# Performance work log

Measured on AMD Instinct MI355X. Metric: run time of the kernel, lower is better.

Reference implementation:

```python
import jax, jax.numpy as jnp
import numpy as np

LBDA = 0.5  # soft-min temperature, default in OTAM_cum_dist_v2


def setup_inputs() -> dict:
    key = jax.random.key(0)
    # frame-similarity distances [n_queries, n_support, q_len, s_len];
    # in the repo these are 1 - cos_sim, i.e. small non-negative floats
    dists = jnp.abs(jax.random.normal(key, (256, 64, 48, 48), dtype=jnp.float32))
    return {"dists": dists}


def _otam_cum_dist(dists, lbda=LBDA):
    """Faithful vectorized port of OTAM_cum_dist_v2.

    dists: [nq, ns, L, M] -> returns [nq, ns] = cum_dists[:, :, -1, -1]
    The torch code pads the last dim by (1,1) with zeros, then runs a
    soft-DTW-style DP:
      row 0      : running sum along m
      col 0      : stays 0 (never written for l >= 1)
      m == 1     : softmin(prev[0],   prev[1],   cur[0])
      1 < m < -1 : softmin(prev[m-1], cur[m-1])
      m == -1    : softmin(prev[-2],  prev[-1],  cur[-2])
    with softmin(xs) = -lbda * log(sum(exp(-x/lbda))).
    """
    nq, ns, L, M = dists.shape
    B = nq * ns
    d = dists.reshape(B, L, M)
    d = jnp.pad(d, ((0, 0), (0, 0), (1, 1)))  # [B, L, M2], M2 = M + 2
    M2 = M + 2

    # row 0: cum[0, m] = cum[0, m-1] + d[0, m], cum[0, 0] = 0 (d[...,0] is the pad 0)
    row0 = jnp.cumsum(d[:, 0, :], axis=-1)  # [B, M2]

    m_idx = jnp.arange(1, M2)
    # prev[m] participates in the softmin only at the two edge columns
    incl_prev_m = (m_idx == 1) | (m_idx == M2 - 1)  # [M2-1] bool

    def row_step(prev, d_row):
        # prev, d_row: [B, M2]; sequential recurrence along m (cur[m] needs cur[m-1])
        xs = (d_row[:, 1:].T, prev[:, :-1].T, prev[:, 1:].T, incl_prev_m)

        def cell(c_prev, x):
            d_m, p_m1, p_m, inc = x  # [B] each, inc scalar bool
            p_m_eff = jnp.where(inc, p_m, jnp.inf)  # exp(-inf/lbda) = 0 -> excluded
            cand = jnp.stack([p_m1, c_prev, p_m_eff], axis=0)  # [3, B]
            c = d_m - lbda * jax.nn.logsumexp(-cand / lbda, axis=0)
            return c, c

        c0 = jnp.zeros(prev.shape[0], dtype=prev.dtype)  # cur[l, 0] = 0
        _, cur = jax.lax.scan(cell, c0, xs)  # [M2-1, B]
        cur = jnp.concatenate([c0[None, :], cur], axis=0).T  # [B, M2]
        return cur, None

    d_rows = jnp.swapaxes(d, 0, 1)[1:]  # [L-1, B, M2]
    final, _ = jax.lax.scan(row_step, row0, d_rows)  # [B, M2]
    return final[:, -1].reshape(nq, ns)


def reference(dists):
    return _otam_cum_dist(dists, LBDA)
```

## Files before the change

kernel.cpp:

```cpp
#include <hip/hip_runtime.h>


__global__ __launch_bounds__(64, 1) void otam_kernel(const float* __restrict__ dists,
                                                     float* __restrict__ out) {
    const int b = blockIdx.x * 64 + threadIdx.x;
    const float* __restrict__ dp = dists + (size_t)b * (48 * 48);

    double P[49];

    {
        const float4* __restrict__ r4 = reinterpret_cast<const float4*>(dp);
        double run = 1.0;
#pragma unroll
        for (int v = 0; v < 12; ++v) {
            float4 q = r4[v];
            run *= (double)__expf(-2.0f * q.x); P[4 * v + 0] = run;
            run *= (double)__expf(-2.0f * q.y); P[4 * v + 1] = run;
            run *= (double)__expf(-2.0f * q.z); P[4 * v + 2] = run;
            run *= (double)__expf(-2.0f * q.w); P[4 * v + 3] = run;
        }
        P[48] = run;
    }

    for (int l = 1; l < 48; ++l) {
        const float4* __restrict__ r4 = reinterpret_cast<const float4*>(dp + l * 48);
        float a[48];
#pragma unroll
        for (int v = 0; v < 12; ++v) {
            float4 q = r4[v];
            a[4 * v + 0] = __expf(-2.0f * q.x);
            a[4 * v + 1] = __expf(-2.0f * q.y);
            a[4 * v + 2] = __expf(-2.0f * q.z);
            a[4 * v + 3] = __expf(-2.0f * q.w);
        }

        double c = (double)a[0] * (2.0 + P[0]);

#pragma unroll
        for (int m = 2; m <= 48; ++m) {
            double t = (double)a[m - 1] * (c + P[m - 2]);
            P[m - 2] = c;
            c = t;
        }

        double t = c + P[47] + P[48];
        P[47] = c;
        P[48] = t;
    }

    out[b] = (float)(-0.5 * log(P[48]));
}

extern "C" void kernel_launch(void* const* d_in, const int* in_sizes, int n_in,
                              void* d_out, int out_size, void* d_ws, size_t ws_size,
                              hipStream_t stream) {
    const float* dists = (const float*)d_in[0];
    float* out = (float*)d_out;
    otam_kernel<<<dim3(256), dim3(64), 0, stream>>>(dists, out);
}
```

Baseline: 240.5 us.

## Split each DP row across 8 lanes with a shuffle-based linear-recurrence scan

Instead of one thread walking all 48 columns of a problem, each problem is now handled by 8 lanes that each own 6 columns. The serial row recurrence is written as an affine map and combined with a log-step shuffle scan, and the next row is prefetched into registers. The goal is to raise parallelism from 16384 threads in 256 single-wave blocks to 131072 threads and to shorten the serial dependency chain. The cost is extra double-precision multiplies and shuffles per row, and rescaling no longer happens per element.

```diff
diff --git a/kernel.cpp b/kernel.cpp
--- a/kernel.cpp
+++ b/kernel.cpp
@@ -1,54 +1,91 @@
 #include <hip/hip_runtime.h>
 
 
-__global__ __launch_bounds__(64, 1) void otam_kernel(const float* __restrict__ dists,
-                                                     float* __restrict__ out) {
-    const int b = blockIdx.x * 64 + threadIdx.x;
-    const float* __restrict__ dp = dists + (size_t)b * (48 * 48);
+__global__ __launch_bounds__(256, 2) void otam_kernel(const float* __restrict__ dists,
+                                                      float* __restrict__ out) {
+    const int t = blockIdx.x * 256 + threadIdx.x;
+    const int k = t & 7;
+    const int prob = t >> 3;
+    const int lane = threadIdx.x & 63;
 
-    double P[49];
+    const float* __restrict__ dp = dists + (size_t)prob * (48 * 48) + 6 * k;
 
-    {
-        const float4* __restrict__ r4 = reinterpret_cast<const float4*>(dp);
-        double run = 1.0;
+    double P[6];
+    double F49 = 0.0;
+
+    float2 q0 = *reinterpret_cast<const float2*>(dp + 0);
+    float2 q1 = *reinterpret_cast<const float2*>(dp + 2);
+    float2 q2 = *reinterpret_cast<const float2*>(dp + 4);
+
+    for (int l = 0; l < 48; ++l) {
+        const float d0 = q0.x, d1 = q0.y, d2 = q1.x, d3 = q1.y, d4 = q2.x, d5 = q2.y;
+
+        {
+            const float* np = dp + (l < 47 ? (l + 1) : l) * 48;
+            q0 = *reinterpret_cast<const float2*>(np + 0);
+            q1 = *reinterpret_cast<const float2*>(np + 2);
+            q2 = *reinterpret_cast<const float2*>(np + 4);
+        }
+
+        double al[6], be[6];
+        al[0] = (double)__expf(-2.0f * d0);
+        al[1] = (double)__expf(-2.0f * d1);
+        al[2] = (double)__expf(-2.0f * d2);
+        al[3] = (double)__expf(-2.0f * d3);
+        al[4] = (double)__expf(-2.0f * d4);
+        al[5] = (double)__expf(-2.0f * d5);
+
+        double Pold5 = 0.0;
+        if (l == 0) {
+            be[0] = 0.0; be[1] = 0.0; be[2] = 0.0; be[3] = 0.0; be[4] = 0.0; be[5] = 0.0;
+        } else {
+            double Plast = __shfl(P[5], (lane - 1) & 63);
+            double pfirst = (k == 0) ? (1.0 + P[0]) : Plast;
+            be[0] = al[0] * pfirst;
+            be[1] = al[1] * P[0];
+            be[2] = al[2] * P[1];
+            be[3] = al[3] * P[2];
+            be[4] = al[4] * P[3];
+            be[5] = al[5] * P[4];
+            Pold5 = P[5];
+        }
+
+        double A = al[0], B = be[0];
 #pragma unroll
-        for (int v = 0; v < 12; ++v) {
-            float4 q = r4[v];
-            run *= (double)__expf(-2.0f * q.x); P[4 * v + 0] = run;
-            run *= (double)__expf(-2.0f * q.y); P[4 * v + 1] = run;
-            run *= (double)__expf(-2.0f * q.z); P[4 * v + 2] = run;
-            run *= (double)__expf(-2.0f * q.w); P[4 * v + 3] = run;
+        for (int i = 1; i < 6; ++i) {
+            B = al[i] * B + be[i];
+            A = al[i] * A;
         }
-        P[48] = run;
+
+#pragma unroll
+        for (int s = 1; s <= 4; s <<= 1) {
+            double Ap = __shfl(A, (lane - s) & 63);
+            double Bp = __shfl(B, (lane - s) & 63);
+            Ap = (k >= s) ? Ap : 1.0;
+            Bp = (k >= s) ? Bp : 0.0;
+            B = A * Bp + B;
+            A = A * Ap;
+        }
+
+        double tAB = A + B;
+        double yin = __shfl(tAB, (lane - 1) & 63);
+        yin = (k == 0) ? 1.0 : yin;
+
+        double y = yin;
+#pragma unroll
+        for (int i = 0; i < 6; ++i) {
+            y = al[i] * y + be[i];
+            P[i] = y;
+        }
+
+        if (k == 7) {
+            F49 = (l == 0) ? y : (y + Pold5 + F49);
+        }
     }
 
-    for (int l = 1; l < 48; ++l) {
-        const float4* __restrict__ r4 = reinterpret_cast<const float4*>(dp + l * 48);
-        float a[48];
-#pragma unroll
-        for (int v = 0; v < 12; ++v) {
-            float4 q = r4[v];
-            a[4 * v + 0] = __expf(-2.0f * q.x);
-            a[4 * v + 1] = __expf(-2.0f * q.y);
-            a[4 * v + 2] = __expf(-2.0f * q.z);
-            a[4 * v + 3] = __expf(-2.0f * q.w);
-        }
-
-        double c = (double)a[0] * (2.0 + P[0]);
-
-#pragma unroll
-        for (int m = 2; m <= 48; ++m) {
-            double t = (double)a[m - 1] * (c + P[m - 2]);
-            P[m - 2] = c;
-            c = t;
-        }
-
-        double t = c + P[47] + P[48];
-        P[47] = c;
-        P[48] = t;
+    if (k == 7) {
+        out[prob] = (float)(-0.5 * log(F49));
     }
-
-    out[b] = (float)(-0.5 * log(P[48]));
 }
 
 extern "C" void kernel_launch(void* const* d_in, const int* in_sizes, int n_in,
@@ -56,5 +93,5 @@
                               hipStream_t stream) {
     const float* dists = (const float*)d_in[0];
     float* out = (float*)d_out;
-    otam_kernel<<<dim3(256), dim3(64), 0, stream>>>(dists, out);
+    otam_kernel<<<dim3(512), dim3(256), 0, stream>>>(dists, out);
 }
```

Result: faster. 216.4 us (-10.0%).

## Parallelize each DP row across 16 lanes with shuffle-based linear-recurrence scan

Applied to the files above, without the earlier changes.

Each problem previously ran on a single thread with a serial 48-step double-precision recurrence per row. The new code gives each problem 16 lanes that own 3 columns each. Each row's first-order linear recurrence is solved with a Hillis-Steele scan of (A,B) affine pairs over wavefront shuffles, in float32 with per-row power-of-two rescaling and a tracked exponent offset. It also prefetches the next row's loads and launches 16x more threads. The risks are float32 precision loss, plus the shuffle and rescaling overhead on every row.

```diff
diff --git a/kernel.cpp b/kernel.cpp
--- a/kernel.cpp
+++ b/kernel.cpp
@@ -1,54 +1,105 @@
 #include <hip/hip_runtime.h>
 
 
-__global__ __launch_bounds__(64, 1) void otam_kernel(const float* __restrict__ dists,
-                                                     float* __restrict__ out) {
-    const int b = blockIdx.x * 64 + threadIdx.x;
-    const float* __restrict__ dp = dists + (size_t)b * (48 * 48);
+__global__ __launch_bounds__(256, 4) void otam_kernel(const float* __restrict__ dists,
+                                                      float* __restrict__ out) {
+    const int t = blockIdx.x * 256 + threadIdx.x;
+    const int k = t & 15;
+    const int prob = t >> 4;
+    const int lane = threadIdx.x & 63;
 
-    double P[49];
+    const float* __restrict__ dp = dists + (size_t)prob * (48 * 48) + 3 * k;
+
+    float P0, P1, P2;
+    float F49 = 0.0f;
+    float S = 1.0f;
+    int offE = 0;
+
+    float q0 = dp[0], q1 = dp[1], q2 = dp[2];
 
     {
-        const float4* __restrict__ r4 = reinterpret_cast<const float4*>(dp);
-        double run = 1.0;
+        float a0 = __expf(-2.0f * q0);
+        float a1 = __expf(-2.0f * q1);
+        float a2 = __expf(-2.0f * q2);
+        q0 = dp[48]; q1 = dp[49]; q2 = dp[50];
+
+        float Ap0 = a0, Ap1 = a0 * a1, Ap2 = a0 * a1 * a2;
+        float A = Ap2;
 #pragma unroll
-        for (int v = 0; v < 12; ++v) {
-            float4 q = r4[v];
-            run *= (double)__expf(-2.0f * q.x); P[4 * v + 0] = run;
-            run *= (double)__expf(-2.0f * q.y); P[4 * v + 1] = run;
-            run *= (double)__expf(-2.0f * q.z); P[4 * v + 2] = run;
-            run *= (double)__expf(-2.0f * q.w); P[4 * v + 3] = run;
+        for (int s = 1; s <= 8; s <<= 1) {
+            float Au = __shfl(A, (lane - s) & 63);
+            A *= (k >= s) ? Au : 1.0f;
         }
-        P[48] = run;
+        float yin = __shfl(A, (lane - 1) & 63);
+        yin = (k == 0) ? 1.0f : yin;
+        P0 = Ap0 * yin; P1 = Ap1 * yin; P2 = Ap2 * yin;
+        F49 = P2;
+    }
+
+    {
+        float m = fmaxf(P0, fmaxf(P1, P2));
+#pragma unroll
+        for (int s = 1; s <= 8; s <<= 1) m = fmaxf(m, __shfl_xor(m, s));
+        unsigned e = (__float_as_uint(m) >> 23) & 0xFFu;
+        float sc = __uint_as_float((254u - e) << 23);
+        offE += (int)e - 127;
+        P0 *= sc; P1 *= sc; P2 *= sc; F49 *= sc; S *= sc;
     }
 
     for (int l = 1; l < 48; ++l) {
-        const float4* __restrict__ r4 = reinterpret_cast<const float4*>(dp + l * 48);
-        float a[48];
-#pragma unroll
-        for (int v = 0; v < 12; ++v) {
-            float4 q = r4[v];
-            a[4 * v + 0] = __expf(-2.0f * q.x);
-            a[4 * v + 1] = __expf(-2.0f * q.y);
-            a[4 * v + 2] = __expf(-2.0f * q.z);
-            a[4 * v + 3] = __expf(-2.0f * q.w);
+        float a0 = __expf(-2.0f * q0);
+        float a1 = __expf(-2.0f * q1);
+        float a2 = __expf(-2.0f * q2);
+
+        {
+            const float* np = dp + (l < 47 ? (l + 1) : l) * 48;
+            q0 = np[0]; q1 = np[1]; q2 = np[2];
         }
 
-        double c = (double)a[0] * (2.0 + P[0]);
+        float Plast = __shfl(P2, (lane - 1) & 63);
+        float pfirst = (k == 0) ? (S + P0) : Plast;
+        float be0 = a0 * pfirst;
+        float be1 = a1 * P0;
+        float be2 = a2 * P1;
+        float PoldLast = P2;
 
+        float Ap0 = a0,        Bp0 = be0;
+        float Ap1 = a1 * Ap0,  Bp1 = fmaf(a1, Bp0, be1);
+        float Ap2 = a2 * Ap1,  Bp2 = fmaf(a2, Bp1, be2);
+
+        float A = Ap2, B = Bp2;
 #pragma unroll
-        for (int m = 2; m <= 48; ++m) {
-            double t = (double)a[m - 1] * (c + P[m - 2]);
-            P[m - 2] = c;
-            c = t;
+        for (int s = 1; s <= 8; s <<= 1) {
+            float Au = __shfl(A, (lane - s) & 63);
+            float Bu = __shfl(B, (lane - s) & 63);
+            Au = (k >= s) ? Au : 1.0f;
+            Bu = (k >= s) ? Bu : 0.0f;
+            B = fmaf(A, Bu, B);
+            A *= Au;
         }
 
-        double t = c + P[47] + P[48];
-        P[47] = c;
-        P[48] = t;
+        float incl = fmaf(A, S, B);
+        float yin = __shfl(incl, (lane - 1) & 63);
+        yin = (k == 0) ? S : yin;
+
+        P0 = fmaf(Ap0, yin, Bp0);
+        P1 = fmaf(Ap1, yin, Bp1);
+        P2 = fmaf(Ap2, yin, Bp2);
+
+        if (k == 15) F49 = P2 + PoldLast + F49;
+
+        float m = fmaxf(P0, fmaxf(P1, P2));
+#pragma unroll
+        for (int s = 1; s <= 8; s <<= 1) m = fmaxf(m, __shfl_xor(m, s));
+        unsigned e = (__float_as_uint(m) >> 23) & 0xFFu;
+        float sc = __uint_as_float((254u - e) << 23);
+        offE += (int)e - 127;
+        P0 *= sc; P1 *= sc; P2 *= sc; F49 *= sc; S *= sc;
     }
 
-    out[b] = (float)(-0.5 * log(P[48]));
+    if (k == 15) {
+        out[prob] = -0.5f * (logf(F49) + (float)offE * 0.6931471805599453f);
+    }
 }
 
 extern "C" void kernel_launch(void* const* d_in, const int* in_sizes, int n_in,
@@ -56,5 +107,5 @@
                               hipStream_t stream) {
     const float* dists = (const float*)d_in[0];
     float* out = (float*)d_out;
-    otam_kernel<<<dim3(256), dim3(64), 0, stream>>>(dists, out);
+    otam_kernel<<<dim3(1024), dim3(256), 0, stream>>>(dists, out);
 }
```

Measured after the change: 211.7 us. -11.9%, faster.

## Parallelize DP rows across 16 lanes with DPP affine scan and float renormalization

Applied to the files above, without the earlier changes.

Replaces the one-thread-per-problem double-precision recurrence with 16 lanes per problem. Each lane owns 4 columns, and each row's linear recurrence is solved as an affine prefix scan using DPP row shifts. Precision drops from double to float, with periodic power-of-two renormalization every four rows to prevent underflow, and row loads are prefetched one block ahead. This raises parallelism from 16K threads to 256K threads and removes slow FP64 work. The cost is extra scan arithmetic and cross-lane ops, plus a numerical risk from float accumulation.

```diff
diff --git a/kernel.cpp b/kernel.cpp
--- a/kernel.cpp
+++ b/kernel.cpp
@@ -1,54 +1,123 @@
 #include <hip/hip_runtime.h>
 
 
-__global__ __launch_bounds__(64, 1) void otam_kernel(const float* __restrict__ dists,
-                                                     float* __restrict__ out) {
-    const int b = blockIdx.x * 64 + threadIdx.x;
-    const float* __restrict__ dp = dists + (size_t)b * (48 * 48);
+template<int CTRL>
+__device__ __forceinline__ float dpp_mov(float src, float old) {
+    return __int_as_float(__builtin_amdgcn_update_dpp(
+        __float_as_int(old), __float_as_int(src), CTRL, 0xF, 0xF, false));
+}
 
-    double P[49];
+__global__ __launch_bounds__(256, 4) void otam_kernel(const float* __restrict__ dists,
+                                                      float* __restrict__ out) {
+    const int t = blockIdx.x * 256 + threadIdx.x;
+    const int k = t & 15;
+    const int prob = t >> 4;
+
+    const float* __restrict__ base =
+        dists + (size_t)prob * 2304 + ((k < 12) ? 4 * k : 0);
+
+    float P0, P1, P2, P3;
+    float F49 = 0.0f;
+    float S = 1.0f;
+    int offE = 0;
+
+    auto do_row = [&](float4 q) {
+        float a0 = __expf(-2.0f * q.x);
+        float a1 = __expf(-2.0f * q.y);
+        float a2 = __expf(-2.0f * q.z);
+        float a3 = __expf(-2.0f * q.w);
+
+        float Plast = dpp_mov<0x111>(P3, 0.0f);
+        float pfirst = (k == 0) ? (S + P0) : Plast;
+        float be0 = a0 * pfirst;
+        float be1 = a1 * P0;
+        float be2 = a2 * P1;
+        float be3 = a3 * P2;
+        float PoldLast = P3;
+
+        float Ap0 = a0,       Bp0 = be0;
+        float Ap1 = a1 * Ap0, Bp1 = fmaf(a1, Bp0, be1);
+        float Ap2 = a2 * Ap1, Bp2 = fmaf(a2, Bp1, be2);
+        float Ap3 = a3 * Ap2, Bp3 = fmaf(a3, Bp2, be3);
+
+        float A = Ap3, B = Bp3;
+        { float Au = dpp_mov<0x111>(A, 1.0f), Bu = dpp_mov<0x111>(B, 0.0f);
+          B = fmaf(A, Bu, B); A *= Au; }
+        { float Au = dpp_mov<0x112>(A, 1.0f), Bu = dpp_mov<0x112>(B, 0.0f);
+          B = fmaf(A, Bu, B); A *= Au; }
+        { float Au = dpp_mov<0x114>(A, 1.0f), Bu = dpp_mov<0x114>(B, 0.0f);
+          B = fmaf(A, Bu, B); A *= Au; }
+        { float Au = dpp_mov<0x118>(A, 1.0f), Bu = dpp_mov<0x118>(B, 0.0f);
+          B = fmaf(A, Bu, B); A *= Au; }
+
+        float incl = fmaf(A, S, B);
+        float yin = dpp_mov<0x111>(incl, S);
+
+        P0 = fmaf(Ap0, yin, Bp0);
+        P1 = fmaf(Ap1, yin, Bp1);
+        P2 = fmaf(Ap2, yin, Bp2);
+        P3 = fmaf(Ap3, yin, Bp3);
+
+        F49 = P3 + PoldLast + F49;
+    };
+
+    auto renorm = [&]() {
+        float m = (k < 12) ? fmaxf(fmaxf(P0, P1), fmaxf(P2, P3)) : 0.0f;
+        m = fmaxf(m, dpp_mov<0x111>(m, 0.0f));
+        m = fmaxf(m, dpp_mov<0x112>(m, 0.0f));
+        m = fmaxf(m, dpp_mov<0x114>(m, 0.0f));
+        m = fmaxf(m, dpp_mov<0x118>(m, 0.0f));
+        float g = __int_as_float(__builtin_amdgcn_ds_swizzle(__float_as_int(m), 0x170));
+        unsigned e = (__float_as_uint(g) >> 23) & 0xFFu;
+        float sc = __uint_as_float((254u - e) << 23);
+        offE += (int)e - 127;
+        P0 *= sc; P1 *= sc; P2 *= sc; P3 *= sc; F49 *= sc; S *= sc;
+    };
+
+    float4 c0 = *(const float4*)(base);
+    float4 c1 = *(const float4*)(base + 48);
+    float4 c2 = *(const float4*)(base + 96);
+    float4 c3 = *(const float4*)(base + 144);
+    float4 n0 = *(const float4*)(base + 192);
+    float4 n1 = *(const float4*)(base + 240);
+    float4 n2 = *(const float4*)(base + 288);
+    float4 n3 = *(const float4*)(base + 336);
 
     {
-        const float4* __restrict__ r4 = reinterpret_cast<const float4*>(dp);
-        double run = 1.0;
-#pragma unroll
-        for (int v = 0; v < 12; ++v) {
-            float4 q = r4[v];
-            run *= (double)__expf(-2.0f * q.x); P[4 * v + 0] = run;
-            run *= (double)__expf(-2.0f * q.y); P[4 * v + 1] = run;
-            run *= (double)__expf(-2.0f * q.z); P[4 * v + 2] = run;
-            run *= (double)__expf(-2.0f * q.w); P[4 * v + 3] = run;
-        }
-        P[48] = run;
+        float a0 = __expf(-2.0f * c0.x);
+        float a1 = __expf(-2.0f * c0.y);
+        float a2 = __expf(-2.0f * c0.z);
+        float a3 = __expf(-2.0f * c0.w);
+        float Ap0 = a0, Ap1 = Ap0 * a1, Ap2 = Ap1 * a2, Ap3 = Ap2 * a3;
+        float A = Ap3;
+        A *= dpp_mov<0x111>(A, 1.0f);
+        A *= dpp_mov<0x112>(A, 1.0f);
+        A *= dpp_mov<0x114>(A, 1.0f);
+        A *= dpp_mov<0x118>(A, 1.0f);
+        float yin = dpp_mov<0x111>(A, 1.0f);
+        P0 = Ap0 * yin; P1 = Ap1 * yin; P2 = Ap2 * yin; P3 = Ap3 * yin;
+        F49 = P3;
+    }
+    do_row(c1); do_row(c2); do_row(c3);
+    renorm();
+    c0 = n0; c1 = n1; c2 = n2; c3 = n3;
+
+    for (int b = 1; b <= 10; ++b) {
+        const float* nb = base + (4 * b + 4) * 48;
+        n0 = *(const float4*)(nb);
+        n1 = *(const float4*)(nb + 48);
+        n2 = *(const float4*)(nb + 96);
+        n3 = *(const float4*)(nb + 144);
+        do_row(c0); do_row(c1); do_row(c2); do_row(c3);
+        renorm();
+        c0 = n0; c1 = n1; c2 = n2; c3 = n3;
     }
 
-    for (int l = 1; l < 48; ++l) {
-        const float4* __restrict__ r4 = reinterpret_cast<const float4*>(dp + l * 48);
-        float a[48];
-#pragma unroll
-        for (int v = 0; v < 12; ++v) {
-            float4 q = r4[v];
-            a[4 * v + 0] = __expf(-2.0f * q.x);
-            a[4 * v + 1] = __expf(-2.0f * q.y);
-            a[4 * v + 2] = __expf(-2.0f * q.z);
-            a[4 * v + 3] = __expf(-2.0f * q.w);
-        }
+    do_row(c0); do_row(c1); do_row(c2); do_row(c3);
 
-        double c = (double)a[0] * (2.0 + P[0]);
-
-#pragma unroll
-        for (int m = 2; m <= 48; ++m) {
-            double t = (double)a[m - 1] * (c + P[m - 2]);
-            P[m - 2] = c;
-            c = t;
-        }
-
-        double t = c + P[47] + P[48];
-        P[47] = c;
-        P[48] = t;
+    if (k == 11) {
+        out[prob] = -0.5f * (logf(F49) + (float)offE * 0.6931471805599453f);
     }
-
-    out[b] = (float)(-0.5 * log(P[48]));
 }
 
 extern "C" void kernel_launch(void* const* d_in, const int* in_sizes, int n_in,
@@ -56,5 +125,5 @@
                               hipStream_t stream) {
     const float* dists = (const float*)d_in[0];
     float* out = (float*)d_out;
-    otam_kernel<<<dim3(256), dim3(64), 0, stream>>>(dists, out);
+    otam_kernel<<<dim3(1024), dim3(256), 0, stream>>>(dists, out);
 }
```

Result: faster. 210.8 us (-12.3%).
